# Kernel tuning notes

Measured on AMD Instinct MI355X. Metric: run time of the kernel, lower is better.

Reference implementation:

```python
import jax, jax.numpy as jnp
import numpy as np

TEMP = 0.05          # args.temp_lp_loss
NUM_CLASSES = 256

def _l2norm(x):
    return x / jnp.linalg.norm(x, axis=-1, keepdims=True)

def setup_inputs() -> dict:
    key = jax.random.key(0)
    k1, k2, k3 = jax.random.split(key, 3)
    B, C, Bs, TOPK = 2048, 2048, 4096, 4
    feats = _l2norm(jax.random.normal(k1, (B, C), jnp.float32))
    feats_s = _l2norm(jax.random.normal(k2, (Bs, TOPK, C), jnp.float32))
    labels = jax.random.randint(k3, (B,), 0, NUM_CLASSES, dtype=jnp.int32)
    # every class 0..255 appears, so each query has >=1 positive support
    labels_s = jnp.arange(Bs * TOPK, dtype=jnp.int32) % NUM_CLASSES
    return {"feats": feats, "feats_s": feats_s, "labels": labels, "labels_s": labels_s}

def reference(feats, feats_s, labels, labels_s):
    Bs, topk, C = feats_s.shape
    fs = feats_s.reshape(Bs * topk, C)                    # [N, C]
    E = jnp.exp(jnp.einsum('bc,nc->bn', feats, fs) / TEMP)  # [B, N]
    is_pos = labels[:, None] == labels_s[None, :]          # [B, N]
    # per-row hardest positive (min over positives of exp-sim)
    pos_min = jnp.min(jnp.where(is_pos, E, jnp.inf), axis=1)   # [B]
    # sum over all negatives of exp-sim
    neg_sum = jnp.sum(jnp.where(is_pos, 0.0, E), axis=1)       # [B]
    loss = -jnp.log(pos_min / (pos_min + neg_sum + 1e-6) + 1e-6)
    return jnp.mean(loss)
```

## Files before the change

kernel.cpp:

```cpp
#include <hip/hip_runtime.h>
#include <hip/hip_bf16.h>
#include <stdint.h>

#define M_TOTAL 2048
#define N_TOTAL 16384
#define K_TOTAL 2048
#define NPARTS  256

#define SCALE_E8M0 0x76767676
#define SCALE_F 512.0f

typedef __attribute__((ext_vector_type(4))) int   int4v;
typedef __attribute__((ext_vector_type(8))) int   int8v;
typedef __attribute__((ext_vector_type(4))) float floatx4;

__global__ void cvt_fp8(const float4* __restrict__ src, uint32_t* __restrict__ dst, int n4) {
    int i = blockIdx.x * blockDim.x + threadIdx.x;
    const int stride = gridDim.x * blockDim.x;
    for (; i < n4; i += stride) {
        float4 v = src[i];
        int p = __builtin_amdgcn_cvt_pk_fp8_f32(v.x * SCALE_F, v.y * SCALE_F, 0, 0);
        p = __builtin_amdgcn_cvt_pk_fp8_f32(v.z * SCALE_F, v.w * SCALE_F, p, 1);
        dst[i] = (uint32_t)p;
    }
}

__device__ __forceinline__ void load16(const void* g, void* l) {
    __builtin_amdgcn_global_load_lds(
        (const __attribute__((address_space(1))) void*)g,
        (__attribute__((address_space(3))) void*)l, 16, 0, 0);
}

__global__ __launch_bounds__(256) void gemm_lp(
        const char* __restrict__ Af8, const char* __restrict__ Bf8,
        const int* __restrict__ labels, const int* __restrict__ labels_s,
        float* __restrict__ pminp, float* __restrict__ psump) {
    __shared__ __align__(16) char lsA[128 * 128];
    __shared__ __align__(16) char lsB[128 * 128];
    __shared__ int lab_m[128];
    __shared__ int lab_n[128];

    const int t    = threadIdx.x;
    const int lane = t & 63;
    const int wave = t >> 6;
    const int wm   = wave >> 1;
    const int wn   = wave & 1;
    const int m0   = blockIdx.y * 128;
    const int n0   = blockIdx.x * 128;

    if (t < 128) lab_m[t] = labels[m0 + t];
    else         lab_n[t - 128] = labels_s[n0 + t - 128];

    const int rq = t >> 3;
    const int qt = (t & 7) ^ ((t >> 3) & 7);
    const char* aPtr = Af8 + (long)(m0 + rq) * K_TOTAL + qt * 16;
    const char* bPtr = Bf8 + (long)(n0 + rq) * K_TOTAL + qt * 16;
    char* lA = lsA + wave * 1024;
    char* lB = lsB + wave * 1024;

    const int quad = lane >> 4;
    const int lcol = lane & 15;
    const int plo = ((2 * quad) ^ (lcol & 7)) << 4;
    const int phi = ((2 * quad + 1) ^ (lcol & 7)) << 4;
    const char* aLo = lsA + (wm * 64 + lcol) * 128 + plo;
    const char* aHi = lsA + (wm * 64 + lcol) * 128 + phi;
    const char* bLo = lsB + (wn * 64 + lcol) * 128 + plo;
    const char* bHi = lsB + (wn * 64 + lcol) * 128 + phi;

    floatx4 acc[4][4];
#pragma unroll
    for (int mi = 0; mi < 4; ++mi)
#pragma unroll
        for (int ni = 0; ni < 4; ++ni)
            acc[mi][ni] = (floatx4){0.f, 0.f, 0.f, 0.f};

#pragma unroll 1
    for (int kt = 0; kt < K_TOTAL / 128; ++kt) {
        __syncthreads();
#pragma unroll
        for (int j = 0; j < 4; ++j) {
            load16(aPtr + j * 32 * K_TOTAL, lA + j * 4096);
            load16(bPtr + j * 32 * K_TOTAL, lB + j * 4096);
        }
        aPtr += 128;
        bPtr += 128;
        __syncthreads();

        int8v bv[4];
#pragma unroll
        for (int i = 0; i < 4; ++i) {
            int4v lo = *(const int4v*)(bLo + i * 2048);
            int4v hi = *(const int4v*)(bHi + i * 2048);
            bv[i] = (int8v){lo.x, lo.y, lo.z, lo.w, hi.x, hi.y, hi.z, hi.w};
        }
#pragma unroll
        for (int mi = 0; mi < 4; ++mi) {
            int4v lo = *(const int4v*)(aLo + mi * 2048);
            int4v hi = *(const int4v*)(aHi + mi * 2048);
            int8v av = (int8v){lo.x, lo.y, lo.z, lo.w, hi.x, hi.y, hi.z, hi.w};
#pragma unroll
            for (int ni = 0; ni < 4; ++ni)
                acc[mi][ni] = __builtin_amdgcn_mfma_scale_f32_16x16x128_f8f6f4(
                    av, bv[ni], acc[mi][ni],
                    0, 0,
                    0, SCALE_E8M0,
                    0, SCALE_E8M0);
        }
    }

    const float scale = 28.853900817779268f;
#pragma unroll
    for (int mi = 0; mi < 4; ++mi) {
#pragma unroll
        for (int r = 0; r < 4; ++r) {
            const int row_local = wm * 64 + mi * 16 + quad * 4 + r;
            const int lab = lab_m[row_local];
            float minv = __builtin_inff();
            float sumv = 0.f;
#pragma unroll
            for (int ni = 0; ni < 4; ++ni) {
                const int col_local = wn * 64 + ni * 16 + lcol;
                const float e = exp2f(acc[mi][ni][r] * scale);
                const bool pos = (lab_n[col_local] == lab);
                minv = pos ? fminf(minv, e) : minv;
                sumv = pos ? sumv : (sumv + e);
            }
#pragma unroll
            for (int off = 1; off < 16; off <<= 1) {
                minv = fminf(minv, __shfl_xor(minv, off, 16));
                sumv += __shfl_xor(sumv, off, 16);
            }
            if (lcol == 0) {
                const long idx = (long)(m0 + row_local) * NPARTS + blockIdx.x * 2 + wn;
                pminp[idx] = minv;
                psump[idx] = sumv;
            }
        }
    }
}

__global__ __launch_bounds__(256) void reduce_rows(
        const float* __restrict__ pminp, const float* __restrict__ psump,
        float* __restrict__ loss) {
    const int row  = blockIdx.x * 4 + (threadIdx.x >> 6);
    const int lane = threadIdx.x & 63;
    float m = __builtin_inff();
    float s = 0.f;
#pragma unroll
    for (int k = 0; k < NPARTS / 64; ++k) {
        const long j = (long)row * NPARTS + lane + k * 64;
        m = fminf(m, pminp[j]);
        s += psump[j];
    }
#pragma unroll
    for (int off = 1; off < 64; off <<= 1) {
        m = fminf(m, __shfl_xor(m, off, 64));
        s += __shfl_xor(s, off, 64);
    }
    if (lane == 0) loss[row] = -logf(m / (m + s + 1e-6f) + 1e-6f);
}

__global__ void final_mean(const float* __restrict__ loss, float* __restrict__ out) {
    float s = 0.f;
    for (int i = threadIdx.x; i < M_TOTAL; i += 256) s += loss[i];
#pragma unroll
    for (int off = 32; off > 0; off >>= 1) s += __shfl_xor(s, off, 64);
    __shared__ float wsum[4];
    if ((threadIdx.x & 63) == 0) wsum[threadIdx.x >> 6] = s;
    __syncthreads();
    if (threadIdx.x == 0)
        out[0] = (wsum[0] + wsum[1] + wsum[2] + wsum[3]) * (1.0f / (float)M_TOTAL);
}

extern "C" void kernel_launch(void* const* d_in, const int* in_sizes, int n_in,
                              void* d_out, int out_size, void* d_ws, size_t ws_size,
                              hipStream_t stream) {
    const float* feats    = (const float*)d_in[0];
    const float* feats_s  = (const float*)d_in[1];
    const int*   labels   = (const int*)d_in[2];
    const int*   labels_s = (const int*)d_in[3];
    float*       out      = (float*)d_out;

    char* ws = (char*)d_ws;
    char*  Af8   = ws;
    char*  Bf8   = ws + 4194304;
    float* pminp = (float*)(ws + 37748736);
    float* psump = (float*)(ws + 39845888);
    float* loss  = (float*)(ws + 41943040);

    cvt_fp8<<<512,  256, 0, stream>>>((const float4*)feats,   (uint32_t*)Af8,
                                      M_TOTAL * K_TOTAL / 4);
    cvt_fp8<<<2048, 256, 0, stream>>>((const float4*)feats_s, (uint32_t*)Bf8,
                                      N_TOTAL * K_TOTAL / 4);

    dim3 grid(N_TOTAL / 128, M_TOTAL / 128);
    gemm_lp<<<grid, 256, 0, stream>>>(Af8, Bf8, labels, labels_s, pminp, psump);

    reduce_rows<<<512, 256, 0, stream>>>(pminp, psump, loss);
    final_mean<<<1, 256, 0, stream>>>(loss, out);
}
```

Before: 289.5 us.

## Double-buffer LDS tiles so global loads overlap MFMA compute

Splits the shared-memory A and B tiles into two buffers. The loop now issues the async global-to-LDS loads for the next K tile before computing on the current one, and processes two K tiles per iteration. The goal is to hide global load latency behind the MFMA work instead of stalling on a barrier every tile. In exchange, LDS use per block doubles, which may lower how many blocks fit on a CU.

New measurement: 307.3 us. 6.1% more time.

```diff
diff --git a/kernel.cpp b/kernel.cpp
--- a/kernel.cpp
+++ b/kernel.cpp
@@ -35,8 +35,8 @@
         const char* __restrict__ Af8, const char* __restrict__ Bf8,
         const int* __restrict__ labels, const int* __restrict__ labels_s,
         float* __restrict__ pminp, float* __restrict__ psump) {
-    __shared__ __align__(16) char lsA[128 * 128];
-    __shared__ __align__(16) char lsB[128 * 128];
+    __shared__ __align__(16) char lsA[2][128 * 128];
+    __shared__ __align__(16) char lsB[2][128 * 128];
     __shared__ int lab_m[128];
     __shared__ int lab_n[128];
 
@@ -55,17 +55,14 @@
     const int qt = (t & 7) ^ ((t >> 3) & 7);
     const char* aPtr = Af8 + (long)(m0 + rq) * K_TOTAL + qt * 16;
     const char* bPtr = Bf8 + (long)(n0 + rq) * K_TOTAL + qt * 16;
-    char* lA = lsA + wave * 1024;
-    char* lB = lsB + wave * 1024;
+    const int ldsOff = wave * 1024;
 
     const int quad = lane >> 4;
     const int lcol = lane & 15;
     const int plo = ((2 * quad) ^ (lcol & 7)) << 4;
     const int phi = ((2 * quad + 1) ^ (lcol & 7)) << 4;
-    const char* aLo = lsA + (wm * 64 + lcol) * 128 + plo;
-    const char* aHi = lsA + (wm * 64 + lcol) * 128 + phi;
-    const char* bLo = lsB + (wn * 64 + lcol) * 128 + plo;
-    const char* bHi = lsB + (wn * 64 + lcol) * 128 + phi;
+    const int aRow = (wm * 64 + lcol) * 128;
+    const int bRow = (wn * 64 + lcol) * 128;
 
     floatx4 acc[4][4];
 #pragma unroll
@@ -74,39 +71,53 @@
         for (int ni = 0; ni < 4; ++ni)
             acc[mi][ni] = (floatx4){0.f, 0.f, 0.f, 0.f};
 
+#define ISSUE_LOADS(tile, p)                                                  \
+    do {                                                                      \
+        _Pragma("unroll")                                                     \
+        for (int j = 0; j < 4; ++j) {                                         \
+            load16(aPtr + (tile) * 128 + j * 32 * K_TOTAL, lsA[p] + ldsOff + j * 4096); \
+            load16(bPtr + (tile) * 128 + j * 32 * K_TOTAL, lsB[p] + ldsOff + j * 4096); \
+        }                                                                     \
+    } while (0)
+
+#define COMPUTE(p)                                                            \
+    do {                                                                      \
+        int8v bv[4];                                                          \
+        _Pragma("unroll")                                                     \
+        for (int i = 0; i < 4; ++i) {                                         \
+            int4v lo = *(const int4v*)(lsB[p] + bRow + i * 2048 + plo);       \
+            int4v hi = *(const int4v*)(lsB[p] + bRow + i * 2048 + phi);       \
+            bv[i] = (int8v){lo.x, lo.y, lo.z, lo.w, hi.x, hi.y, hi.z, hi.w};  \
+        }                                                                     \
+        _Pragma("unroll")                                                     \
+        for (int mi = 0; mi < 4; ++mi) {                                      \
+            int4v lo = *(const int4v*)(lsA[p] + aRow + mi * 2048 + plo);      \
+            int4v hi = *(const int4v*)(lsA[p] + aRow + mi * 2048 + phi);      \
+            int8v av = (int8v){lo.x, lo.y, lo.z, lo.w, hi.x, hi.y, hi.z, hi.w}; \
+            _Pragma("unroll")                                                 \
+            for (int ni = 0; ni < 4; ++ni)                                    \
+                acc[mi][ni] = __builtin_amdgcn_mfma_scale_f32_16x16x128_f8f6f4( \
+                    av, bv[ni], acc[mi][ni], 0, 0,                            \
+                    0, SCALE_E8M0, 0, SCALE_E8M0);                            \
+        }                                                                     \
+    } while (0)
+
+    ISSUE_LOADS(0, 0);
+
 #pragma unroll 1
-    for (int kt = 0; kt < K_TOTAL / 128; ++kt) {
+    for (int kt2 = 0; kt2 < K_TOTAL / 256; ++kt2) {
         __syncthreads();
-#pragma unroll
-        for (int j = 0; j < 4; ++j) {
-            load16(aPtr + j * 32 * K_TOTAL, lA + j * 4096);
-            load16(bPtr + j * 32 * K_TOTAL, lB + j * 4096);
-        }
-        aPtr += 128;
-        bPtr += 128;
+        ISSUE_LOADS(1, 1);
+        COMPUTE(0);
         __syncthreads();
-
-        int8v bv[4];
-#pragma unroll
-        for (int i = 0; i < 4; ++i) {
-            int4v lo = *(const int4v*)(bLo + i * 2048);
-            int4v hi = *(const int4v*)(bHi + i * 2048);
-            bv[i] = (int8v){lo.x, lo.y, lo.z, lo.w, hi.x, hi.y, hi.z, hi.w};
-        }
-#pragma unroll
-        for (int mi = 0; mi < 4; ++mi) {
-            int4v lo = *(const int4v*)(aLo + mi * 2048);
-            int4v hi = *(const int4v*)(aHi + mi * 2048);
-            int8v av = (int8v){lo.x, lo.y, lo.z, lo.w, hi.x, hi.y, hi.z, hi.w};
-#pragma unroll
-            for (int ni = 0; ni < 4; ++ni)
-                acc[mi][ni] = __builtin_amdgcn_mfma_scale_f32_16x16x128_f8f6f4(
-                    av, bv[ni], acc[mi][ni],
-                    0, 0,
-                    0, SCALE_E8M0,
-                    0, SCALE_E8M0);
-        }
-    }
+        if (kt2 < K_TOTAL / 256 - 1)
+            ISSUE_LOADS(2, 0);
+        COMPUTE(1);
+        aPtr += 256;
+        bPtr += 256;
+    }
+#undef ISSUE_LOADS
+#undef COMPUTE
 
     const float scale = 28.853900817779268f;
 #pragma unroll
```
